# Optimization experiments

Measured on AMD Instinct MI355X. Metric: run time of the kernel, lower is better.

Reference implementation:

```python
import jax, jax.numpy as jnp
import numpy as np

NUM_HOPS = 3
SIGMA = 0.1
EPS = 1e-12  # torch F.normalize default eps


def setup_inputs() -> dict:
    key = jax.random.key(0)
    k1, k2 = jax.random.split(key)
    N, D, E = 50000, 128, 800000
    x = jax.random.normal(k1, (N, D), dtype=jnp.float32)
    edge_index = jax.random.randint(k2, (2, E), 0, N, dtype=jnp.int64)
    return {"x": x, "edge_index": edge_index}


def _l2_normalize(h):
    # matches torch.nn.functional.normalize(x, dim=1)
    n = jnp.linalg.norm(h, axis=1, keepdims=True)
    return h / jnp.maximum(n, EPS)


def reference(x, edge_index):
    N = x.shape[0]
    src, dst = edge_index[0], edge_index[1]
    noise_keys = jax.random.split(jax.random.key(1), NUM_HOPS)

    h = _l2_normalize(x)
    outs = [h]
    for k in range(NUM_HOPS):
        # edge-wise inner-product similarity + sigmoid gate
        e = jnp.sum(h[src] * h[dst], axis=1)          # [E]
        alpha = jax.nn.sigmoid(e)                     # [E]
        # sparse alpha^T @ h == segment-sum over dst of alpha * h[src]
        aggr = jax.ops.segment_sum(alpha[:, None] * h[src], dst, num_segments=N)  # [N, D]
        noised = aggr + SIGMA * jax.random.normal(noise_keys[k], aggr.shape, dtype=x.dtype)
        h = _l2_normalize(noised)
        outs.append(h)
    return jnp.stack(outs)                            # [NUM_HOPS+1, N, D]
```

## Files before the change

kernel.cpp:

```cpp
#include <hip/hip_runtime.h>
#include <cstdint>
#include <cstddef>

#define D 128

typedef float v2f __attribute__((ext_vector_type(2)));

__host__ __device__ inline uint32_t rotl32(uint32_t v, int d) {
  return (v << d) | (v >> (32 - d));
}

__host__ __device__ inline void threefry2x32(uint32_t k0, uint32_t k1,
                                             uint32_t x0, uint32_t x1,
                                             uint32_t* o0, uint32_t* o1) {
  uint32_t k2 = k0 ^ k1 ^ 0x1BD11BDAu;
  x0 += k0; x1 += k1;
#define TF_RND(r) x0 += x1; x1 = rotl32(x1, (r)); x1 ^= x0;
  TF_RND(13) TF_RND(15) TF_RND(26) TF_RND(6)
  x0 += k1; x1 += k2 + 1u;
  TF_RND(17) TF_RND(29) TF_RND(16) TF_RND(24)
  x0 += k2; x1 += k0 + 2u;
  TF_RND(13) TF_RND(15) TF_RND(26) TF_RND(6)
  x0 += k0; x1 += k1 + 3u;
  TF_RND(17) TF_RND(29) TF_RND(16) TF_RND(24)
  x0 += k1; x1 += k2 + 4u;
  TF_RND(13) TF_RND(15) TF_RND(26) TF_RND(6)
  x0 += k2; x1 += k0 + 5u;
#undef TF_RND
  *o0 = x0; *o1 = x1;
}

__device__ inline float erfinv_f32(float x) {
  float w = -log1pf(-x * x);
  float p;
  if (w < 5.0f) {
    w = w - 2.5f;
    p = 2.81022636e-08f;
    p = fmaf(p, w, 3.43273939e-07f);
    p = fmaf(p, w, -3.5233877e-06f);
    p = fmaf(p, w, -4.39150654e-06f);
    p = fmaf(p, w, 0.00021858087f);
    p = fmaf(p, w, -0.00125372503f);
    p = fmaf(p, w, -0.00417768164f);
    p = fmaf(p, w, 0.246640727f);
    p = fmaf(p, w, 1.50140941f);
  } else {
    w = sqrtf(w) - 3.0f;
    p = -0.000200214257f;
    p = fmaf(p, w, 0.000100950558f);
    p = fmaf(p, w, 0.00134934322f);
    p = fmaf(p, w, -0.00367342844f);
    p = fmaf(p, w, 0.00573950773f);
    p = fmaf(p, w, -0.0076224613f);
    p = fmaf(p, w, 0.00943887047f);
    p = fmaf(p, w, 1.00167406f);
    p = fmaf(p, w, 2.83297682f);
  }
  return p * x;
}

__device__ inline float erfinv_fast(float x) {
  float t = fmaf(-x, x, 1.0f);
  float w = -0.693147180559945f * __builtin_amdgcn_logf(t);
  float p;
  if (__builtin_expect(w < 5.0f, 1)) {
    w = w - 2.5f;
    p = 2.81022636e-08f;
    p = fmaf(p, w, 3.43273939e-07f);
    p = fmaf(p, w, -3.5233877e-06f);
    p = fmaf(p, w, -4.39150654e-06f);
    p = fmaf(p, w, 0.00021858087f);
    p = fmaf(p, w, -0.00125372503f);
    p = fmaf(p, w, -0.00417768164f);
    p = fmaf(p, w, 0.246640727f);
    p = fmaf(p, w, 1.50140941f);
  } else {
    w = __builtin_amdgcn_sqrtf(w) - 3.0f;
    p = -0.000200214257f;
    p = fmaf(p, w, 0.000100950558f);
    p = fmaf(p, w, 0.00134934322f);
    p = fmaf(p, w, -0.00367342844f);
    p = fmaf(p, w, 0.00573950773f);
    p = fmaf(p, w, -0.0076224613f);
    p = fmaf(p, w, 0.00943887047f);
    p = fmaf(p, w, 1.00167406f);
    p = fmaf(p, w, 2.83297682f);
  }
  return p * x;
}

__device__ inline float jax_normal_elem(uint32_t k0, uint32_t k1, uint32_t idx) {
  uint32_t o0, o1;
  threefry2x32(k0, k1, 0u, idx, &o0, &o1);
  uint32_t bits = o0 ^ o1;
  float f = __uint_as_float((bits >> 9) | 0x3F800000u) - 1.0f;
  float u = f * 2.0f + (-0.99999994f);
  u = fmaxf(-0.99999994f, u);
  return 1.41421356237309505f * erfinv_f32(u);
}

__device__ inline float jax_normal_fast(uint32_t k0, uint32_t k1, uint32_t idx) {
  uint32_t o0, o1;
  threefry2x32(k0, k1, 0u, idx, &o0, &o1);
  uint32_t bits = o0 ^ o1;
  float f = __uint_as_float((bits >> 9) | 0x3F800000u) - 1.0f;
  float u = f * 2.0f + (-0.99999994f);
  u = fmaxf(-0.99999994f, u);
  return 1.41421356237309505f * erfinv_fast(u);
}

__device__ inline uint32_t f32_to_bf16_rne(float f) {
  uint32_t u = __float_as_uint(f);
  u += 0x7fffu + ((u >> 16) & 1u);
  return u >> 16;
}

__device__ inline void gen_noise8(float* __restrict__ np, size_t NDl, int k,
                                  uint32_t k0, uint32_t k1) {
  size_t base = ((size_t)k * 256 + threadIdx.x) * 8;
  if (base + 8 <= NDl) {
    float vv[8];
#pragma unroll
    for (int i = 0; i < 8; ++i)
      vv[i] = 0.1f * jax_normal_fast(k0, k1, (uint32_t)base + (uint32_t)i);
    float4* q = (float4*)(np + base);
    q[0] = make_float4(vv[0], vv[1], vv[2], vv[3]);
    q[1] = make_float4(vv[4], vv[5], vv[6], vv[7]);
  }
}

__device__ inline bool role_split(int bid, int s, int Z, int* work, int* nz) {
  int k = bid / s;
  int r = bid - k * s;
  if (r == s - 1 && k < Z) { *nz = k; return true; }
  *work = bid - min(k, Z);
  return false;
}

__global__ __launch_bounds__(256) void front_kernel(
    const int* __restrict__ dst, int* __restrict__ counts,
    int* __restrict__ deg_hist, int E4, int E,
    const float* __restrict__ xin, float* __restrict__ out0,
    uint16_t* __restrict__ mir, int N,
    float* __restrict__ noise0, int s, int Z, int nbHist,
    uint32_t k0, uint32_t k1) {
  int w, nz;
  if (role_split(blockIdx.x, s, Z, &w, &nz)) {
    gen_noise8(noise0, (size_t)N * D, nz, k0, k1);
    return;
  }
  if (w < nbHist) {
    if (w == 0) {
      for (int bb = threadIdx.x; bb < 1024; bb += 256) deg_hist[bb] = 0;
    }
    int t = w * 256 + threadIdx.x;
    if (t < E4) {
      int4 d4 = ((const int4*)dst)[t];
      atomicAdd(&counts[d4.x], 1);
      atomicAdd(&counts[d4.y], 1);
      atomicAdd(&counts[d4.z], 1);
      atomicAdd(&counts[d4.w], 1);
    }
    int rem = E4 * 4 + t;
    if (t < E - E4 * 4) atomicAdd(&counts[dst[rem]], 1);
    return;
  }
  int t = (w - nbHist) * 256 + threadIdx.x;
  int row = t >> 6;
  int lane = t & 63;
  if (row >= N) return;
  size_t base = (size_t)row * D + 2 * lane;
  float2 v = *(const float2*)(xin + base);
  float ss = v.x * v.x + v.y * v.y;
#pragma unroll
  for (int off = 32; off > 0; off >>= 1) ss += __shfl_xor(ss, off);
  float denom = fmaxf(sqrtf(ss), 1e-12f);
  float2 o = make_float2(v.x / denom, v.y / denom);
  *(float2*)(out0 + base) = o;
  if (mir) {
    uint32_t wq = f32_to_bf16_rne(o.x) | (f32_to_bf16_rne(o.y) << 16);
    *(uint32_t*)(mir + base) = wq;
  }
}

__global__ __launch_bounds__(256) void scanA_kernel(
    int* __restrict__ counts, int* __restrict__ blocksums,
    int* __restrict__ deg, int* __restrict__ deg_hist, int N) {
  __shared__ int tmp[256];
  __shared__ int lhist[1024];
  for (int b = threadIdx.x; b < 1024; b += 256) lhist[b] = 0;
  int tid = threadIdx.x;
  int i = blockIdx.x * 256 + tid;
  int v = (i < N) ? counts[i] : 0;
  tmp[tid] = v;
  __syncthreads();
  if (i < N) {
    deg[i] = v;
    atomicAdd(&lhist[min(v, 1023)], 1);
  }
  for (int off = 1; off < 256; off <<= 1) {
    int t = (tid >= off) ? tmp[tid - off] : 0;
    __syncthreads();
    tmp[tid] += t;
    __syncthreads();
  }
  if (i < N) counts[i] = tmp[tid] - v;
  if (tid == 255) blocksums[blockIdx.x] = tmp[tid];
  __syncthreads();
  for (int b = threadIdx.x; b < 1024; b += 256) {
    int c = lhist[b];
    if (c) atomicAdd(&deg_hist[b], c);
  }
}

__global__ __launch_bounds__(256) void scanB_kernel(
    int* __restrict__ blocksums, int nb,
    const int* __restrict__ deg_hist, int* __restrict__ deg_cursor) {
  __shared__ int tmp[256];
  int tid = threadIdx.x;
  int v = (tid < nb) ? blocksums[tid] : 0;
  tmp[tid] = v;
  __syncthreads();
  for (int off = 1; off < 256; off <<= 1) {
    int t = (tid >= off) ? tmp[tid - off] : 0;
    __syncthreads();
    tmp[tid] += t;
    __syncthreads();
  }
  if (tid < nb) blocksums[tid] = tmp[tid] - v;
  __syncthreads();
  int loc[4], s = 0;
#pragma unroll
  for (int k = 0; k < 4; ++k) { loc[k] = deg_hist[tid * 4 + k]; s += loc[k]; }
  __syncthreads();
  tmp[tid] = s;
  __syncthreads();
  for (int off = 1; off < 256; off <<= 1) {
    int t = (tid >= off) ? tmp[tid - off] : 0;
    __syncthreads();
    tmp[tid] += t;
    __syncthreads();
  }
  int run = tmp[tid] - s;
#pragma unroll
  for (int k = 0; k < 4; ++k) { deg_cursor[tid * 4 + k] = run; run += loc[k]; }
}

__global__ __launch_bounds__(256) void scanC_kernel(
    int* __restrict__ offsets, int* __restrict__ cursor,
    const int* __restrict__ blocksums, const int* __restrict__ deg,
    int* __restrict__ deg_cursor, int* __restrict__ perm, int N, int E) {
  __shared__ int lhist[1024];
  __shared__ int lbase[1024];
  for (int b = threadIdx.x; b < 1024; b += 256) lhist[b] = 0;
  __syncthreads();
  int i = blockIdx.x * 256 + threadIdx.x;
  int d = 0, lpos = 0;
  if (i < N) {
    int o = offsets[i] + blocksums[blockIdx.x];
    offsets[i] = o;
    cursor[i] = o;
    d = min(deg[i], 1023);
    lpos = atomicAdd(&lhist[d], 1);
  }
  if (i == 0) offsets[N] = E;
  __syncthreads();
  for (int b = threadIdx.x; b < 1024; b += 256) {
    int c = lhist[b];
    lbase[b] = c ? atomicAdd(&deg_cursor[b], c) : 0;
  }
  __syncthreads();
  if (i < N) perm[lbase[d] + lpos] = i;
}

__global__ __launch_bounds__(256) void edgescatter4_kernel(
    const int* __restrict__ src, const int* __restrict__ dst,
    int* __restrict__ cursor, int* __restrict__ sorted_src, int E4, int E) {
  int t = blockIdx.x * blockDim.x + threadIdx.x;
  if (t < E4) {
    int4 d = ((const int4*)dst)[t];
    int4 s = ((const int4*)src)[t];
    sorted_src[atomicAdd(&cursor[d.x], 1)] = s.x;
    sorted_src[atomicAdd(&cursor[d.y], 1)] = s.y;
    sorted_src[atomicAdd(&cursor[d.z], 1)] = s.z;
    sorted_src[atomicAdd(&cursor[d.w], 1)] = s.w;
  }
  int rem = E4 * 4 + t;
  if (t < E - E4 * 4) {
    int d = dst[rem];
    sorted_src[atomicAdd(&cursor[d], 1)] = src[rem];
  }
}

union V8 { float4 v[2]; v2f d[4]; float f[8]; };
union U4B { uint4 v; uint32_t u[4]; };

__device__ inline void hop_edge_pk(const U4B& raw, const V8& b, V8& acc) {
  V8 af;
#pragma unroll
  for (int i = 0; i < 4; ++i) {
    af.f[2 * i] = __uint_as_float(raw.u[i] << 16);
    af.f[2 * i + 1] = __uint_as_float(raw.u[i] & 0xffff0000u);
  }
  v2f p2 = af.d[0] * b.d[0];
#pragma unroll
  for (int q = 1; q < 4; ++q) p2 = __builtin_elementwise_fma(af.d[q], b.d[q], p2);
  float part = p2.x + p2.y;
  part += __shfl_xor(part, 1);
  part += __shfl_xor(part, 2);
  part += __shfl_xor(part, 4);
  part += __shfl_xor(part, 8);
  float alpha = __builtin_amdgcn_rcpf(1.0f + __expf(-part));
  v2f av = { alpha, alpha };
#pragma unroll
  for (int q = 0; q < 4; ++q) acc.d[q] = __builtin_elementwise_fma(av, af.d[q], acc.d[q]);
}

__global__ __launch_bounds__(256, 4) void hop_kernel_bf16_pre(
    const float* __restrict__ hprev, const uint16_t* __restrict__ mprev,
    float* __restrict__ hout, uint16_t* __restrict__ mout,
    const int* __restrict__ offsets, const int* __restrict__ sorted_src,
    const int* __restrict__ perm, const float* __restrict__ noise,
    float* __restrict__ noiseNext, int s, int Z,
    uint32_t nk0, uint32_t nk1, int N, int E) {
  int w, nz;
  if (role_split(blockIdx.x, s, Z, &w, &nz)) {
    gen_noise8(noiseNext, (size_t)N * D, nz, nk0, nk1);
    return;
  }
  int g = w * 16 + (threadIdx.x >> 4);
  int sub = threadIdx.x & 15;
  if (g >= N) return;
  int r = perm[g];
  size_t rbase = (size_t)r * D + sub * 8;

  V8 b;
  {
    const float4* p = (const float4*)(hprev + rbase);
    b.v[0] = p[0]; b.v[1] = p[1];
  }
  V8 acc;
#pragma unroll
  for (int i = 0; i < 8; ++i) acc.f[i] = 0.f;

  int j0 = offsets[r];
  int cnt = offsets[r + 1] - j0;
  int Em1 = E - 1;
  const char* mb = (const char*)mprev + (uint32_t)(sub * 16);

  U4B buf[4];
  int sNext[4];
#pragma unroll
  for (int q = 0; q < 4; ++q) {
    uint32_t sidx = (uint32_t)sorted_src[min(j0 + q, Em1)];
    buf[q].v = *(const uint4*)(mb + (sidx << 8));
  }
#pragma unroll
  for (int q = 0; q < 4; ++q) sNext[q] = sorted_src[min(j0 + 4 + q, Em1)];

  int cnt4 = cnt & ~3;
  for (int i = 0; i < cnt4; i += 4) {
#pragma unroll
    for (int q = 0; q < 4; ++q) {
      hop_edge_pk(buf[q], b, acc);
      buf[q].v = *(const uint4*)(mb + ((uint32_t)sNext[q] << 8));
      sNext[q] = sorted_src[min(j0 + i + 8 + q, Em1)];
    }
  }
  int rem = cnt - cnt4;
#pragma unroll
  for (int q = 0; q < 3; ++q)
    if (q < rem) hop_edge_pk(buf[q], b, acc);

  V8 nzv;
  {
    const float4* p = (const float4*)(noise + rbase);
    nzv.v[0] = p[0]; nzv.v[1] = p[1];
  }
  float ss = 0.f;
#pragma unroll
  for (int i2 = 0; i2 < 8; ++i2) {
    acc.f[i2] += nzv.f[i2];
    ss = fmaf(acc.f[i2], acc.f[i2], ss);
  }
  ss += __shfl_xor(ss, 1);
  ss += __shfl_xor(ss, 2);
  ss += __shfl_xor(ss, 4);
  ss += __shfl_xor(ss, 8);
  float denom = fmaxf(sqrtf(ss), 1e-12f);
  float inv = __builtin_amdgcn_rcpf(denom);
  inv = inv * fmaf(-denom, inv, 2.0f);
#pragma unroll
  for (int i2 = 0; i2 < 8; ++i2) acc.f[i2] *= inv;
  {
    float4* p = (float4*)(hout + rbase);
    p[0] = acc.v[0]; p[1] = acc.v[1];
  }
  if (mout) {
    U4B wq;
#pragma unroll
    for (int i2 = 0; i2 < 4; ++i2)
      wq.u[i2] = f32_to_bf16_rne(acc.f[2 * i2]) |
                 (f32_to_bf16_rne(acc.f[2 * i2 + 1]) << 16);
    *(uint4*)(mout + rbase) = wq.v;
  }
}

__device__ inline void hop_edge(const U4B& raw, const V8& b, V8& acc) {
  V8 af;
#pragma unroll
  for (int i = 0; i < 4; ++i) {
    af.f[2 * i] = __uint_as_float(raw.u[i] << 16);
    af.f[2 * i + 1] = __uint_as_float(raw.u[i] & 0xffff0000u);
  }
  float part = af.f[0] * b.f[0];
#pragma unroll
  for (int q = 1; q < 8; ++q) part = fmaf(af.f[q], b.f[q], part);
  part += __shfl_xor(part, 1);
  part += __shfl_xor(part, 2);
  part += __shfl_xor(part, 4);
  part += __shfl_xor(part, 8);
  float alpha = __builtin_amdgcn_rcpf(1.0f + __expf(-part));
#pragma unroll
  for (int q = 0; q < 8; ++q) acc.f[q] = fmaf(alpha, af.f[q], acc.f[q]);
}

__global__ __launch_bounds__(256, 4) void hop_kernel_bf16(
    const float* __restrict__ hprev, const uint16_t* __restrict__ mprev,
    float* __restrict__ hout, uint16_t* __restrict__ mout,
    const int* __restrict__ offsets, const int* __restrict__ sorted_src,
    const int* __restrict__ perm, int N, int E, uint32_t k0, uint32_t k1) {
  int g = (blockIdx.x * blockDim.x + threadIdx.x) >> 4;
  int sub = threadIdx.x & 15;
  if (g >= N) return;
  int r = perm[g];
  size_t rbase = (size_t)r * D + sub * 8;

  V8 b;
  {
    const float4* p = (const float4*)(hprev + rbase);
    b.v[0] = p[0]; b.v[1] = p[1];
  }
  V8 acc;
#pragma unroll
  for (int i = 0; i < 8; ++i) acc.f[i] = 0.f;

  int j0 = offsets[r];
  int cnt = offsets[r + 1] - j0;
  int Em1 = E - 1;
  const uint16_t* mp = mprev + sub * 8;

  U4B buf[4];
  int sNext[4];
#pragma unroll
  for (int q = 0; q < 4; ++q) {
    int s = sorted_src[min(j0 + q, Em1)];
    buf[q].v = *(const uint4*)(mp + (size_t)s * D);
  }
#pragma unroll
  for (int q = 0; q < 4; ++q) sNext[q] = sorted_src[min(j0 + 4 + q, Em1)];

  int cnt4 = cnt & ~3;
  int i = 0;
  for (; i < cnt4; i += 4) {
#pragma unroll
    for (int q = 0; q < 4; ++q) {
      hop_edge(buf[q], b, acc);
      buf[q].v = *(const uint4*)(mp + (size_t)sNext[q] * D);
      sNext[q] = sorted_src[min(j0 + i + 8 + q, Em1)];
    }
  }
  int rem = cnt - cnt4;
#pragma unroll
  for (int q = 0; q < 3; ++q)
    if (q < rem) hop_edge(buf[q], b, acc);

  uint32_t idx = (uint32_t)rbase;
  float ss = 0.f;
#pragma unroll
  for (int i2 = 0; i2 < 8; ++i2) {
    acc.f[i2] += 0.1f * jax_normal_elem(k0, k1, idx + (uint32_t)i2);
    ss = fmaf(acc.f[i2], acc.f[i2], ss);
  }
  ss += __shfl_xor(ss, 1);
  ss += __shfl_xor(ss, 2);
  ss += __shfl_xor(ss, 4);
  ss += __shfl_xor(ss, 8);
  float denom = fmaxf(sqrtf(ss), 1e-12f);
#pragma unroll
  for (int i2 = 0; i2 < 8; ++i2) acc.f[i2] = acc.f[i2] / denom;
  {
    float4* p = (float4*)(hout + rbase);
    p[0] = acc.v[0]; p[1] = acc.v[1];
  }
  if (mout) {
    U4B w;
#pragma unroll
    for (int i2 = 0; i2 < 4; ++i2)
      w.u[i2] = f32_to_bf16_rne(acc.f[2 * i2]) |
                (f32_to_bf16_rne(acc.f[2 * i2 + 1]) << 16);
    *(uint4*)(mout + rbase) = w.v;
  }
}

union V16 { float4 v[4]; float f[16]; };

__global__ __launch_bounds__(256) void hop_kernel_f32(
    const float* __restrict__ hprev, float* __restrict__ hout,
    const int* __restrict__ offsets, const int* __restrict__ sorted_src,
    const int* __restrict__ perm, int N, uint32_t k0, uint32_t k1) {
  int g = (blockIdx.x * blockDim.x + threadIdx.x) >> 3;
  int sub = threadIdx.x & 7;
  if (g >= N) return;
  int r = perm[g];
  size_t rbase = (size_t)r * D + sub * 16;

  V16 b;
  {
    const float4* p = (const float4*)(hprev + rbase);
    b.v[0] = p[0]; b.v[1] = p[1]; b.v[2] = p[2]; b.v[3] = p[3];
  }
  V16 acc;
#pragma unroll
  for (int i = 0; i < 16; ++i) acc.f[i] = 0.f;

  int j = offsets[r], jhi = offsets[r + 1];
  V16 a;
  if (j < jhi) {
    const float4* p = (const float4*)(hprev + (size_t)sorted_src[j] * D + sub * 16);
    a.v[0] = p[0]; a.v[1] = p[1]; a.v[2] = p[2]; a.v[3] = p[3];
  }
  while (j < jhi) {
    int jn = j + 1;
    V16 an;
    if (jn < jhi) {
      const float4* p = (const float4*)(hprev + (size_t)sorted_src[jn] * D + sub * 16);
      an.v[0] = p[0]; an.v[1] = p[1]; an.v[2] = p[2]; an.v[3] = p[3];
    }
    float part = a.f[0] * b.f[0];
#pragma unroll
    for (int i = 1; i < 16; ++i) part = fmaf(a.f[i], b.f[i], part);
    part += __shfl_xor(part, 1);
    part += __shfl_xor(part, 2);
    part += __shfl_xor(part, 4);
    float alpha = 1.0f / (1.0f + expf(-part));
#pragma unroll
    for (int i = 0; i < 16; ++i) acc.f[i] = fmaf(alpha, a.f[i], acc.f[i]);
    a = an;
    j = jn;
  }

  uint32_t idx = (uint32_t)rbase;
  float ss = 0.f;
#pragma unroll
  for (int i = 0; i < 16; ++i) {
    acc.f[i] += 0.1f * jax_normal_elem(k0, k1, idx + (uint32_t)i);
    ss = fmaf(acc.f[i], acc.f[i], ss);
  }
  ss += __shfl_xor(ss, 1);
  ss += __shfl_xor(ss, 2);
  ss += __shfl_xor(ss, 4);
  float denom = fmaxf(sqrtf(ss), 1e-12f);
#pragma unroll
  for (int i = 0; i < 16; ++i) acc.f[i] = acc.f[i] / denom;
  {
    float4* p = (float4*)(hout + rbase);
    p[0] = acc.v[0]; p[1] = acc.v[1]; p[2] = acc.v[2]; p[3] = acc.v[3];
  }
}

extern "C" void kernel_launch(void* const* d_in, const int* in_sizes, int n_in,
                              void* d_out, int out_size, void* d_ws, size_t ws_size,
                              hipStream_t stream) {
  const float* x = (const float*)d_in[0];
  const int* ei = (const int*)d_in[1];
  int N = in_sizes[0] / D;
  int E = in_sizes[1] / 2;
  const int* src = ei;
  const int* dst = ei + E;
  float* out = (float*)d_out;
  size_t ND = (size_t)N * D;

  int nblocksN = (N + 255) / 256;

  int* offsets = (int*)d_ws;
  int* cursor = offsets + (N + 1);
  int* perm = cursor + N;
  int* deg = perm + N;
  int* deg_hist = deg + N;
  int* deg_cursor = deg_hist + 1024;
  int* blocksums = deg_cursor + 1024;
  int* sorted_src = blocksums + 256;
  size_t intWords = (size_t)(N + 1) + N + N + N + 1024 + 1024 + 256 + E;
  size_t mirOff = (intWords * 4 + 255) & ~(size_t)255;
  size_t needMir = mirOff + 2 * ND * sizeof(uint16_t);
  bool use_bf16 = ws_size >= needMir;
  uint16_t* mir0 = (uint16_t*)((char*)d_ws + mirOff);
  uint16_t* mir1 = mir0 + ND;
  size_t noiseOff = needMir;
  size_t needNoise = noiseOff + 3 * ND * sizeof(float);
  bool use_noise = use_bf16 && ws_size >= needNoise;
  float* noisebuf = (float*)((char*)d_ws + noiseOff);

  uint32_t nk0[3], nk1[3];
  for (int k = 0; k < 3; ++k)
    threefry2x32(0u, 1u, 0u, (uint32_t)k, &nk0[k], &nk1[k]);

  int E4 = E / 4;
  int e4Blocks = (max(E4, E - E4 * 4) + 255) / 256;
  int rowWaveBlocks = (int)(((size_t)N * 64 + 255) / 256);
  int hopBlocks16 = (int)(((size_t)N * 16 + 255) / 256);
  int hopBlocks8 = (int)(((size_t)N * 8 + 255) / 256);

  int nbHist = e4Blocks;
  int nbNorm = rowWaveBlocks;
  int Zn = use_noise ? (int)((ND + 2047) / 2048) : 0;

  int WF = nbHist + nbNorm;
  int TF = WF + Zn;
  int sF = Zn ? max(2, TF / Zn) : 1;
  hipMemsetAsync(offsets, 0, (size_t)(N + 1) * sizeof(int), stream);
  hipLaunchKernelGGL(front_kernel, dim3(TF), dim3(256), 0, stream,
                     dst, offsets, deg_hist, E4, E,
                     x, out, use_bf16 ? mir0 : (uint16_t*)nullptr, N,
                     noisebuf, sF, Zn, nbHist, nk0[0], nk1[0]);
  hipLaunchKernelGGL(scanA_kernel, dim3(nblocksN), dim3(256), 0, stream,
                     offsets, blocksums, deg, deg_hist, N);
  hipLaunchKernelGGL(scanB_kernel, dim3(1), dim3(256), 0, stream,
                     blocksums, nblocksN, deg_hist, deg_cursor);
  hipLaunchKernelGGL(scanC_kernel, dim3(nblocksN), dim3(256), 0, stream,
                     offsets, cursor, blocksums, deg, deg_cursor, perm, N, E);
  hipLaunchKernelGGL(edgescatter4_kernel, dim3(e4Blocks), dim3(256), 0, stream,
                     src, dst, cursor, sorted_src, E4, E);

  if (use_bf16) {
    uint16_t* mirs[4] = {mir0, mir1, mir0, nullptr};
    for (int k = 0; k < 3; ++k) {
      const float* hk = out + (size_t)k * ND;
      float* hk1 = out + (size_t)(k + 1) * ND;
      if (use_noise) {
        int ZH = (k < 2) ? Zn : 0;
        int TH = hopBlocks16 + ZH;
        int sH = ZH ? max(2, TH / ZH) : 1;
        float* nNext = (k < 2) ? (noisebuf + (size_t)(k + 1) * ND) : nullptr;
        uint32_t kn0 = (k < 2) ? nk0[k + 1] : 0u;
        uint32_t kn1 = (k < 2) ? nk1[k + 1] : 0u;
        hipLaunchKernelGGL(hop_kernel_bf16_pre, dim3(TH), dim3(256), 0, stream,
                           hk, mirs[k], hk1, mirs[k + 1], offsets, sorted_src,
                           perm, noisebuf + (size_t)k * ND, nNext, sH, ZH,
                           kn0, kn1, N, E);
      } else {
        hipLaunchKernelGGL(hop_kernel_bf16, dim3(hopBlocks16), dim3(256), 0,
                           stream, hk, mirs[k], hk1, mirs[k + 1], offsets,
                           sorted_src, perm, N, E, nk0[k], nk1[k]);
      }
    }
  } else {
    for (int k = 0; k < 3; ++k) {
      const float* hk = out + (size_t)k * ND;
      float* hk1 = out + (size_t)(k + 1) * ND;
      hipLaunchKernelGGL(hop_kernel_f32, dim3(hopBlocks8), dim3(256), 0, stream,
                         hk, hk1, offsets, sorted_src, perm, N, nk0[k], nk1[k]);
    }
  }
}
```

Measured before the change: 388.8 us.

## Fuse whole pipeline into one cooperative persistent kernel with grid syncs

Replaces the sequence of memset, front, three scan, scatter and three hop launches with a single cooperative mega_kernel that uses grid.sync between phases and grid-stride loops over work units. Noise generation for all three hops is interleaved into the histogram and scatter phases. The aim is to remove per-launch overhead and inter-kernel gaps. In exchange, occupancy is limited to what a cooperative launch allows, and grid-wide barriers are added. The old multi-kernel path is kept as a fallback, with small guards added for the no-noise case.

```diff
diff --git a/kernel.cpp b/kernel.cpp
--- a/kernel.cpp
+++ b/kernel.cpp
@@ -1,6 +1,9 @@
 #include <hip/hip_runtime.h>
+#include <hip/hip_cooperative_groups.h>
 #include <cstdint>
 #include <cstddef>
+
+namespace cg = cooperative_groups;
 
 #define D 128
 
@@ -129,12 +132,325 @@
   }
 }
 
+__device__ inline bool mix_role(int u, int T, int Z, int* work, int* nz) {
+  long long a = (long long)u * Z;
+  int before = (int)(a / T);
+  int after = (int)((a + Z) / T);
+  if (after > before) { *nz = before; return true; }
+  *work = u - before;
+  return false;
+}
+
 __device__ inline bool role_split(int bid, int s, int Z, int* work, int* nz) {
   int k = bid / s;
   int r = bid - k * s;
   if (r == s - 1 && k < Z) { *nz = k; return true; }
   *work = bid - min(k, Z);
   return false;
+}
+
+union V8 { float4 v[2]; v2f d[4]; float f[8]; };
+union U4B { uint4 v; uint32_t u[4]; };
+
+__device__ inline void hop_edge_pk(const U4B& raw, const V8& b, V8& acc) {
+  V8 af;
+#pragma unroll
+  for (int i = 0; i < 4; ++i) {
+    af.f[2 * i] = __uint_as_float(raw.u[i] << 16);
+    af.f[2 * i + 1] = __uint_as_float(raw.u[i] & 0xffff0000u);
+  }
+  v2f p2 = af.d[0] * b.d[0];
+#pragma unroll
+  for (int q = 1; q < 4; ++q) p2 = __builtin_elementwise_fma(af.d[q], b.d[q], p2);
+  float part = p2.x + p2.y;
+  part += __shfl_xor(part, 1);
+  part += __shfl_xor(part, 2);
+  part += __shfl_xor(part, 4);
+  part += __shfl_xor(part, 8);
+  float alpha = __builtin_amdgcn_rcpf(1.0f + __expf(-part));
+  v2f av = { alpha, alpha };
+#pragma unroll
+  for (int q = 0; q < 4; ++q) acc.d[q] = __builtin_elementwise_fma(av, af.d[q], acc.d[q]);
+}
+
+__device__ inline void hop_unit(int g, const float* __restrict__ hprev,
+    const uint16_t* __restrict__ mprev, float* __restrict__ hout,
+    uint16_t* __restrict__ mout, const int* __restrict__ offsets,
+    const int* __restrict__ sorted_src, const int* __restrict__ perm,
+    const float* __restrict__ noise, int N, int E) {
+  int sub = threadIdx.x & 15;
+  if (g >= N) return;
+  int r = perm[g];
+  size_t rbase = (size_t)r * D + sub * 8;
+
+  V8 b;
+  {
+    const float4* p = (const float4*)(hprev + rbase);
+    b.v[0] = p[0]; b.v[1] = p[1];
+  }
+  V8 acc;
+#pragma unroll
+  for (int i = 0; i < 8; ++i) acc.f[i] = 0.f;
+
+  int j0 = offsets[r];
+  int cnt = offsets[r + 1] - j0;
+  int Em1 = E - 1;
+  const char* mb = (const char*)mprev + (uint32_t)(sub * 16);
+
+  U4B buf[4];
+  int sNext[4];
+#pragma unroll
+  for (int q = 0; q < 4; ++q) {
+    uint32_t s = (uint32_t)sorted_src[min(j0 + q, Em1)];
+    buf[q].v = *(const uint4*)(mb + (s << 8));
+  }
+#pragma unroll
+  for (int q = 0; q < 4; ++q) sNext[q] = sorted_src[min(j0 + 4 + q, Em1)];
+
+  int cnt4 = cnt & ~3;
+  for (int i = 0; i < cnt4; i += 4) {
+#pragma unroll
+    for (int q = 0; q < 4; ++q) {
+      hop_edge_pk(buf[q], b, acc);
+      buf[q].v = *(const uint4*)(mb + ((uint32_t)sNext[q] << 8));
+      sNext[q] = sorted_src[min(j0 + i + 8 + q, Em1)];
+    }
+  }
+  int rem = cnt - cnt4;
+#pragma unroll
+  for (int q = 0; q < 3; ++q)
+    if (q < rem) hop_edge_pk(buf[q], b, acc);
+
+  V8 nzv;
+  {
+    const float4* p = (const float4*)(noise + rbase);
+    nzv.v[0] = p[0]; nzv.v[1] = p[1];
+  }
+  float ss = 0.f;
+#pragma unroll
+  for (int i2 = 0; i2 < 8; ++i2) {
+    acc.f[i2] += nzv.f[i2];
+    ss = fmaf(acc.f[i2], acc.f[i2], ss);
+  }
+  ss += __shfl_xor(ss, 1);
+  ss += __shfl_xor(ss, 2);
+  ss += __shfl_xor(ss, 4);
+  ss += __shfl_xor(ss, 8);
+  float denom = fmaxf(sqrtf(ss), 1e-12f);
+  float inv = __builtin_amdgcn_rcpf(denom);
+  inv = inv * fmaf(-denom, inv, 2.0f);
+#pragma unroll
+  for (int i2 = 0; i2 < 8; ++i2) acc.f[i2] *= inv;
+  {
+    float4* p = (float4*)(hout + rbase);
+    p[0] = acc.v[0]; p[1] = acc.v[1];
+  }
+  if (mout) {
+    U4B wq;
+#pragma unroll
+    for (int i2 = 0; i2 < 4; ++i2)
+      wq.u[i2] = f32_to_bf16_rne(acc.f[2 * i2]) |
+                 (f32_to_bf16_rne(acc.f[2 * i2 + 1]) << 16);
+    *(uint4*)(mout + rbase) = wq.v;
+  }
+}
+
+struct MegaArgs {
+  const float* x;
+  const int* src;
+  const int* dst;
+  float* out;
+  int* offsets;
+  int* cursor;
+  int* perm;
+  int* deg;
+  int* deg_hist;
+  int* deg_cursor;
+  int* blocksums;
+  int* sorted_src;
+  uint16_t* mir0;
+  uint16_t* mir1;
+  float* noise;
+  int N, E, E4, nbHist, nbNorm, nbScan, Zn, hopU;
+  uint32_t k0a, k1a, k0b, k1b, k0c, k1c;
+};
+
+__global__ __launch_bounds__(256, 8) void mega_kernel(MegaArgs A) {
+  cg::grid_group grid = cg::this_grid();
+  __shared__ int sh_tmp[256];
+  __shared__ int sh_a[1024];
+  __shared__ int sh_b[1024];
+  const int nb = gridDim.x;
+  const int bid = blockIdx.x;
+  const int tid = threadIdx.x;
+  const size_t NDl = (size_t)A.N * D;
+
+  {
+    int gt = bid * 256 + tid, gs = nb * 256;
+    for (int i = gt; i < A.N + 1; i += gs) A.offsets[i] = 0;
+    for (int i = gt; i < 1024; i += gs) A.deg_hist[i] = 0;
+  }
+  grid.sync();
+
+  {
+    int T = A.nbHist + A.nbNorm + A.Zn;
+    for (int u = bid; u < T; u += nb) {
+      int w, nz;
+      if (mix_role(u, T, A.Zn, &w, &nz)) {
+        gen_noise8(A.noise, NDl, nz, A.k0a, A.k1a);
+      } else if (w < A.nbHist) {
+        int t = w * 256 + tid;
+        if (t < A.E4) {
+          int4 d4 = ((const int4*)A.dst)[t];
+          atomicAdd(&A.offsets[d4.x], 1);
+          atomicAdd(&A.offsets[d4.y], 1);
+          atomicAdd(&A.offsets[d4.z], 1);
+          atomicAdd(&A.offsets[d4.w], 1);
+        }
+        int rem = A.E4 * 4 + t;
+        if (t < A.E - A.E4 * 4) atomicAdd(&A.offsets[A.dst[rem]], 1);
+      } else {
+        int t = (w - A.nbHist) * 256 + tid;
+        int row = t >> 6;
+        int lane = t & 63;
+        if (row < A.N) {
+          size_t base = (size_t)row * D + 2 * lane;
+          float2 v = *(const float2*)(A.x + base);
+          float ss = v.x * v.x + v.y * v.y;
+#pragma unroll
+          for (int off = 32; off > 0; off >>= 1) ss += __shfl_xor(ss, off);
+          float denom = fmaxf(sqrtf(ss), 1e-12f);
+          float2 o = make_float2(v.x / denom, v.y / denom);
+          *(float2*)(A.out + base) = o;
+          uint32_t wq = f32_to_bf16_rne(o.x) | (f32_to_bf16_rne(o.y) << 16);
+          *(uint32_t*)(A.mir0 + base) = wq;
+        }
+      }
+    }
+  }
+  grid.sync();
+
+  for (int vb = bid; vb < A.nbScan; vb += nb) {
+    for (int b2 = tid; b2 < 1024; b2 += 256) sh_a[b2] = 0;
+    int i = vb * 256 + tid;
+    int v = (i < A.N) ? A.offsets[i] : 0;
+    sh_tmp[tid] = v;
+    __syncthreads();
+    if (i < A.N) {
+      A.deg[i] = v;
+      atomicAdd(&sh_a[min(v, 1023)], 1);
+    }
+    for (int off = 1; off < 256; off <<= 1) {
+      int t2 = (tid >= off) ? sh_tmp[tid - off] : 0;
+      __syncthreads();
+      sh_tmp[tid] += t2;
+      __syncthreads();
+    }
+    if (i < A.N) A.offsets[i] = sh_tmp[tid] - v;
+    if (tid == 255) A.blocksums[vb] = sh_tmp[tid];
+    __syncthreads();
+    for (int b2 = tid; b2 < 1024; b2 += 256) {
+      int c = sh_a[b2];
+      if (c) atomicAdd(&A.deg_hist[b2], c);
+    }
+    __syncthreads();
+  }
+  grid.sync();
+
+  if (bid == 0) {
+    int v = (tid < A.nbScan) ? A.blocksums[tid] : 0;
+    sh_tmp[tid] = v;
+    __syncthreads();
+    for (int off = 1; off < 256; off <<= 1) {
+      int t2 = (tid >= off) ? sh_tmp[tid - off] : 0;
+      __syncthreads();
+      sh_tmp[tid] += t2;
+      __syncthreads();
+    }
+    if (tid < A.nbScan) A.blocksums[tid] = sh_tmp[tid] - v;
+    __syncthreads();
+    int loc[4], s = 0;
+#pragma unroll
+    for (int k = 0; k < 4; ++k) { loc[k] = A.deg_hist[tid * 4 + k]; s += loc[k]; }
+    __syncthreads();
+    sh_tmp[tid] = s;
+    __syncthreads();
+    for (int off = 1; off < 256; off <<= 1) {
+      int t2 = (tid >= off) ? sh_tmp[tid - off] : 0;
+      __syncthreads();
+      sh_tmp[tid] += t2;
+      __syncthreads();
+    }
+    int run = sh_tmp[tid] - s;
+#pragma unroll
+    for (int k = 0; k < 4; ++k) { A.deg_cursor[tid * 4 + k] = run; run += loc[k]; }
+  }
+  grid.sync();
+
+  for (int vb = bid; vb < A.nbScan; vb += nb) {
+    for (int b2 = tid; b2 < 1024; b2 += 256) sh_a[b2] = 0;
+    __syncthreads();
+    int i = vb * 256 + tid;
+    int d2 = 0, lpos = 0;
+    if (i < A.N) {
+      int o = A.offsets[i] + A.blocksums[vb];
+      A.offsets[i] = o;
+      A.cursor[i] = o;
+      d2 = min(A.deg[i], 1023);
+      lpos = atomicAdd(&sh_a[d2], 1);
+    }
+    if (i == 0) A.offsets[A.N] = A.E;
+    __syncthreads();
+    for (int b2 = tid; b2 < 1024; b2 += 256) {
+      int c = sh_a[b2];
+      sh_b[b2] = c ? atomicAdd(&A.deg_cursor[b2], c) : 0;
+    }
+    __syncthreads();
+    if (i < A.N) A.perm[sh_b[d2] + lpos] = i;
+    __syncthreads();
+  }
+  grid.sync();
+
+  {
+    int Zs = 2 * A.Zn;
+    int T = A.nbHist + Zs;
+    for (int u = bid; u < T; u += nb) {
+      int w, nz;
+      if (mix_role(u, T, Zs, &w, &nz)) {
+        if (nz < A.Zn) gen_noise8(A.noise + NDl, NDl, nz, A.k0b, A.k1b);
+        else gen_noise8(A.noise + 2 * NDl, NDl, nz - A.Zn, A.k0c, A.k1c);
+      } else {
+        int t = w * 256 + tid;
+        if (t < A.E4) {
+          int4 d4 = ((const int4*)A.dst)[t];
+          int4 s4 = ((const int4*)A.src)[t];
+          A.sorted_src[atomicAdd(&A.cursor[d4.x], 1)] = s4.x;
+          A.sorted_src[atomicAdd(&A.cursor[d4.y], 1)] = s4.y;
+          A.sorted_src[atomicAdd(&A.cursor[d4.z], 1)] = s4.z;
+          A.sorted_src[atomicAdd(&A.cursor[d4.w], 1)] = s4.w;
+        }
+        int rem = A.E4 * 4 + t;
+        if (t < A.E - A.E4 * 4) {
+          int dd = A.dst[rem];
+          A.sorted_src[atomicAdd(&A.cursor[dd], 1)] = A.src[rem];
+        }
+      }
+    }
+  }
+  grid.sync();
+
+  for (int u = bid; u < A.hopU; u += nb)
+    hop_unit(u * 16 + (tid >> 4), A.out, A.mir0, A.out + NDl, A.mir1,
+             A.offsets, A.sorted_src, A.perm, A.noise, A.N, A.E);
+  grid.sync();
+  for (int u = bid; u < A.hopU; u += nb)
+    hop_unit(u * 16 + (tid >> 4), A.out + NDl, A.mir1, A.out + 2 * NDl, A.mir0,
+             A.offsets, A.sorted_src, A.perm, A.noise + NDl, A.N, A.E);
+  grid.sync();
+  for (int u = bid; u < A.hopU; u += nb)
+    hop_unit(u * 16 + (tid >> 4), A.out + 2 * NDl, A.mir0, A.out + 3 * NDl,
+             (uint16_t*)nullptr, A.offsets, A.sorted_src, A.perm,
+             A.noise + 2 * NDl, A.N, A.E);
 }
 
 __global__ __launch_bounds__(256) void front_kernel(
@@ -145,10 +461,11 @@
     float* __restrict__ noise0, int s, int Z, int nbHist,
     uint32_t k0, uint32_t k1) {
   int w, nz;
-  if (role_split(blockIdx.x, s, Z, &w, &nz)) {
+  if (Z > 0 && role_split(blockIdx.x, s, Z, &w, &nz)) {
     gen_noise8(noise0, (size_t)N * D, nz, k0, k1);
     return;
   }
+  if (Z == 0) w = blockIdx.x;
   if (w < nbHist) {
     if (w == 0) {
       for (int bb = threadIdx.x; bb < 1024; bb += 256) deg_hist[bb] = 0;
@@ -292,30 +609,6 @@
   }
 }
 
-union V8 { float4 v[2]; v2f d[4]; float f[8]; };
-union U4B { uint4 v; uint32_t u[4]; };
-
-__device__ inline void hop_edge_pk(const U4B& raw, const V8& b, V8& acc) {
-  V8 af;
-#pragma unroll
-  for (int i = 0; i < 4; ++i) {
-    af.f[2 * i] = __uint_as_float(raw.u[i] << 16);
-    af.f[2 * i + 1] = __uint_as_float(raw.u[i] & 0xffff0000u);
-  }
-  v2f p2 = af.d[0] * b.d[0];
-#pragma unroll
-  for (int q = 1; q < 4; ++q) p2 = __builtin_elementwise_fma(af.d[q], b.d[q], p2);
-  float part = p2.x + p2.y;
-  part += __shfl_xor(part, 1);
-  part += __shfl_xor(part, 2);
-  part += __shfl_xor(part, 4);
-  part += __shfl_xor(part, 8);
-  float alpha = __builtin_amdgcn_rcpf(1.0f + __expf(-part));
-  v2f av = { alpha, alpha };
-#pragma unroll
-  for (int q = 0; q < 4; ++q) acc.d[q] = __builtin_elementwise_fma(av, af.d[q], acc.d[q]);
-}
-
 __global__ __launch_bounds__(256, 4) void hop_kernel_bf16_pre(
     const float* __restrict__ hprev, const uint16_t* __restrict__ mprev,
     float* __restrict__ hout, uint16_t* __restrict__ mout,
@@ -324,183 +617,13 @@
     float* __restrict__ noiseNext, int s, int Z,
     uint32_t nk0, uint32_t nk1, int N, int E) {
   int w, nz;
-  if (role_split(blockIdx.x, s, Z, &w, &nz)) {
+  if (Z > 0 && role_split(blockIdx.x, s, Z, &w, &nz)) {
     gen_noise8(noiseNext, (size_t)N * D, nz, nk0, nk1);
     return;
   }
-  int g = w * 16 + (threadIdx.x >> 4);
-  int sub = threadIdx.x & 15;
-  if (g >= N) return;
-  int r = perm[g];
-  size_t rbase = (size_t)r * D + sub * 8;
-
-  V8 b;
-  {
-    const float4* p = (const float4*)(hprev + rbase);
-    b.v[0] = p[0]; b.v[1] = p[1];
-  }
-  V8 acc;
-#pragma unroll
-  for (int i = 0; i < 8; ++i) acc.f[i] = 0.f;
-
-  int j0 = offsets[r];
-  int cnt = offsets[r + 1] - j0;
-  int Em1 = E - 1;
-  const char* mb = (const char*)mprev + (uint32_t)(sub * 16);
-
-  U4B buf[4];
-  int sNext[4];
-#pragma unroll
-  for (int q = 0; q < 4; ++q) {
-    uint32_t sidx = (uint32_t)sorted_src[min(j0 + q, Em1)];
-    buf[q].v = *(const uint4*)(mb + (sidx << 8));
-  }
-#pragma unroll
-  for (int q = 0; q < 4; ++q) sNext[q] = sorted_src[min(j0 + 4 + q, Em1)];
-
-  int cnt4 = cnt & ~3;
-  for (int i = 0; i < cnt4; i += 4) {
-#pragma unroll
-    for (int q = 0; q < 4; ++q) {
-      hop_edge_pk(buf[q], b, acc);
-      buf[q].v = *(const uint4*)(mb + ((uint32_t)sNext[q] << 8));
-      sNext[q] = sorted_src[min(j0 + i + 8 + q, Em1)];
-    }
-  }
-  int rem = cnt - cnt4;
-#pragma unroll
-  for (int q = 0; q < 3; ++q)
-    if (q < rem) hop_edge_pk(buf[q], b, acc);
-
-  V8 nzv;
-  {
-    const float4* p = (const float4*)(noise + rbase);
-    nzv.v[0] = p[0]; nzv.v[1] = p[1];
-  }
-  float ss = 0.f;
-#pragma unroll
-  for (int i2 = 0; i2 < 8; ++i2) {
-    acc.f[i2] += nzv.f[i2];
-    ss = fmaf(acc.f[i2], acc.f[i2], ss);
-  }
-  ss += __shfl_xor(ss, 1);
-  ss += __shfl_xor(ss, 2);
-  ss += __shfl_xor(ss, 4);
-  ss += __shfl_xor(ss, 8);
-  float denom = fmaxf(sqrtf(ss), 1e-12f);
-  float inv = __builtin_amdgcn_rcpf(denom);
-  inv = inv * fmaf(-denom, inv, 2.0f);
-#pragma unroll
-  for (int i2 = 0; i2 < 8; ++i2) acc.f[i2] *= inv;
-  {
-    float4* p = (float4*)(hout + rbase);
-    p[0] = acc.v[0]; p[1] = acc.v[1];
-  }
-  if (mout) {
-    U4B wq;
-#pragma unroll
-    for (int i2 = 0; i2 < 4; ++i2)
-      wq.u[i2] = f32_to_bf16_rne(acc.f[2 * i2]) |
-                 (f32_to_bf16_rne(acc.f[2 * i2 + 1]) << 16);
-    *(uint4*)(mout + rbase) = wq.v;
-  }
-}
-
-__device__ inline void hop_edge(const U4B& raw, const V8& b, V8& acc) {
-  V8 af;
-#pragma unroll
-  for (int i = 0; i < 4; ++i) {
-    af.f[2 * i] = __uint_as_float(raw.u[i] << 16);
-    af.f[2 * i + 1] = __uint_as_float(raw.u[i] & 0xffff0000u);
-  }
-  float part = af.f[0] * b.f[0];
-#pragma unroll
-  for (int q = 1; q < 8; ++q) part = fmaf(af.f[q], b.f[q], part);
-  part += __shfl_xor(part, 1);
-  part += __shfl_xor(part, 2);
-  part += __shfl_xor(part, 4);
-  part += __shfl_xor(part, 8);
-  float alpha = __builtin_amdgcn_rcpf(1.0f + __expf(-part));
-#pragma unroll
-  for (int q = 0; q < 8; ++q) acc.f[q] = fmaf(alpha, af.f[q], acc.f[q]);
-}
-
-__global__ __launch_bounds__(256, 4) void hop_kernel_bf16(
-    const float* __restrict__ hprev, const uint16_t* __restrict__ mprev,
-    float* __restrict__ hout, uint16_t* __restrict__ mout,
-    const int* __restrict__ offsets, const int* __restrict__ sorted_src,
-    const int* __restrict__ perm, int N, int E, uint32_t k0, uint32_t k1) {
-  int g = (blockIdx.x * blockDim.x + threadIdx.x) >> 4;
-  int sub = threadIdx.x & 15;
-  if (g >= N) return;
-  int r = perm[g];
-  size_t rbase = (size_t)r * D + sub * 8;
-
-  V8 b;
-  {
-    const float4* p = (const float4*)(hprev + rbase);
-    b.v[0] = p[0]; b.v[1] = p[1];
-  }
-  V8 acc;
-#pragma unroll
-  for (int i = 0; i < 8; ++i) acc.f[i] = 0.f;
-
-  int j0 = offsets[r];
-  int cnt = offsets[r + 1] - j0;
-  int Em1 = E - 1;
-  const uint16_t* mp = mprev + sub * 8;
-
-  U4B buf[4];
-  int sNext[4];
-#pragma unroll
-  for (int q = 0; q < 4; ++q) {
-    int s = sorted_src[min(j0 + q, Em1)];
-    buf[q].v = *(const uint4*)(mp + (size_t)s * D);
-  }
-#pragma unroll
-  for (int q = 0; q < 4; ++q) sNext[q] = sorted_src[min(j0 + 4 + q, Em1)];
-
-  int cnt4 = cnt & ~3;
-  int i = 0;
-  for (; i < cnt4; i += 4) {
-#pragma unroll
-    for (int q = 0; q < 4; ++q) {
-      hop_edge(buf[q], b, acc);
-      buf[q].v = *(const uint4*)(mp + (size_t)sNext[q] * D);
-      sNext[q] = sorted_src[min(j0 + i + 8 + q, Em1)];
-    }
-  }
-  int rem = cnt - cnt4;
-#pragma unroll
-  for (int q = 0; q < 3; ++q)
-    if (q < rem) hop_edge(buf[q], b, acc);
-
-  uint32_t idx = (uint32_t)rbase;
-  float ss = 0.f;
-#pragma unroll
-  for (int i2 = 0; i2 < 8; ++i2) {
-    acc.f[i2] += 0.1f * jax_normal_elem(k0, k1, idx + (uint32_t)i2);
-    ss = fmaf(acc.f[i2], acc.f[i2], ss);
-  }
-  ss += __shfl_xor(ss, 1);
-  ss += __shfl_xor(ss, 2);
-  ss += __shfl_xor(ss, 4);
-  ss += __shfl_xor(ss, 8);
-  float denom = fmaxf(sqrtf(ss), 1e-12f);
-#pragma unroll
-  for (int i2 = 0; i2 < 8; ++i2) acc.f[i2] = acc.f[i2] / denom;
-  {
-    float4* p = (float4*)(hout + rbase);
-    p[0] = acc.v[0]; p[1] = acc.v[1];
-  }
-  if (mout) {
-    U4B w;
-#pragma unroll
-    for (int i2 = 0; i2 < 4; ++i2)
-      w.u[i2] = f32_to_bf16_rne(acc.f[2 * i2]) |
-                (f32_to_bf16_rne(acc.f[2 * i2 + 1]) << 16);
-    *(uint4*)(mout + rbase) = w.v;
-  }
+  if (Z == 0) w = blockIdx.x;
+  hop_unit(w * 16 + (threadIdx.x >> 4), hprev, mprev, hout, mout,
+           offsets, sorted_src, perm, noise, N, E);
 }
 
 union V16 { float4 v[4]; float f[16]; };
@@ -611,16 +734,52 @@
   int rowWaveBlocks = (int)(((size_t)N * 64 + 255) / 256);
   int hopBlocks16 = (int)(((size_t)N * 16 + 255) / 256);
   int hopBlocks8 = (int)(((size_t)N * 8 + 255) / 256);
+  int Zn = use_noise ? (int)((ND + 2047) / 2048) : 0;
+
+  static int s_nb = -2;
+  if (s_nb == -2) {
+    s_nb = -1;
+    int devId = 0;
+    if (hipGetDevice(&devId) == hipSuccess) {
+      hipDeviceProp_t prop;
+      if (hipGetDeviceProperties(&prop, devId) == hipSuccess &&
+          prop.cooperativeLaunch) {
+        int maxB = 0;
+        if (hipOccupancyMaxActiveBlocksPerMultiprocessor(&maxB, mega_kernel,
+                                                         256, 0) == hipSuccess &&
+            maxB > 0) {
+          long long g = (long long)maxB * prop.multiProcessorCount;
+          s_nb = (int)(g > 4096 ? 4096 : g);
+        }
+      }
+    }
+  }
+
+  bool try_mega = use_noise && nblocksN <= 256 && s_nb > 0;
+  if (try_mega) {
+    MegaArgs A;
+    A.x = x; A.src = src; A.dst = dst; A.out = out;
+    A.offsets = offsets; A.cursor = cursor; A.perm = perm; A.deg = deg;
+    A.deg_hist = deg_hist; A.deg_cursor = deg_cursor; A.blocksums = blocksums;
+    A.sorted_src = sorted_src; A.mir0 = mir0; A.mir1 = mir1; A.noise = noisebuf;
+    A.N = N; A.E = E; A.E4 = E4; A.nbHist = e4Blocks; A.nbNorm = rowWaveBlocks;
+    A.nbScan = nblocksN; A.Zn = Zn; A.hopU = (N + 15) / 16;
+    A.k0a = nk0[0]; A.k1a = nk1[0];
+    A.k0b = nk0[1]; A.k1b = nk1[1];
+    A.k0c = nk0[2]; A.k1c = nk1[2];
+    void* args[] = { &A };
+    hipError_t cerr = hipLaunchCooperativeKernel(mega_kernel, dim3(s_nb),
+                                                 dim3(256), args, 0, stream);
+    if (cerr == hipSuccess) return;
+  }
 
   int nbHist = e4Blocks;
   int nbNorm = rowWaveBlocks;
-  int Zn = use_noise ? (int)((ND + 2047) / 2048) : 0;
-
   int WF = nbHist + nbNorm;
   int TF = WF + Zn;
   int sF = Zn ? max(2, TF / Zn) : 1;
   hipMemsetAsync(offsets, 0, (size_t)(N + 1) * sizeof(int), stream);
-  hipLaunchKernelGGL(front_kernel, dim3(TF), dim3(256), 0, stream,
+  hipLaunchKernelGGL(front_kernel, dim3(Zn ? TF : WF), dim3(256), 0, stream,
                      dst, offsets, deg_hist, E4, E,
                      x, out, use_bf16 ? mir0 : (uint16_t*)nullptr, N,
                      noisebuf, sF, Zn, nbHist, nk0[0], nk1[0]);
@@ -633,27 +792,22 @@
   hipLaunchKernelGGL(edgescatter4_kernel, dim3(e4Blocks), dim3(256), 0, stream,
                      src, dst, cursor, sorted_src, E4, E);
 
-  if (use_bf16) {
+  if (use_bf16 && use_noise) {
     uint16_t* mirs[4] = {mir0, mir1, mir0, nullptr};
     for (int k = 0; k < 3; ++k) {
       const float* hk = out + (size_t)k * ND;
       float* hk1 = out + (size_t)(k + 1) * ND;
-      if (use_noise) {
-        int ZH = (k < 2) ? Zn : 0;
-        int TH = hopBlocks16 + ZH;
-        int sH = ZH ? max(2, TH / ZH) : 1;
-        float* nNext = (k < 2) ? (noisebuf + (size_t)(k + 1) * ND) : nullptr;
-        uint32_t kn0 = (k < 2) ? nk0[k + 1] : 0u;
-        uint32_t kn1 = (k < 2) ? nk1[k + 1] : 0u;
-        hipLaunchKernelGGL(hop_kernel_bf16_pre, dim3(TH), dim3(256), 0, stream,
-                           hk, mirs[k], hk1, mirs[k + 1], offsets, sorted_src,
-                           perm, noisebuf + (size_t)k * ND, nNext, sH, ZH,
-                           kn0, kn1, N, E);
-      } else {
-        hipLaunchKernelGGL(hop_kernel_bf16, dim3(hopBlocks16), dim3(256), 0,
-                           stream, hk, mirs[k], hk1, mirs[k + 1], offsets,
-                           sorted_src, perm, N, E, nk0[k], nk1[k]);
-      }
+      int ZH = (k < 2) ? Zn : 0;
+      int TH = hopBlocks16 + ZH;
+      int sH = ZH ? max(2, TH / ZH) : 1;
+      float* nNext = (k < 2) ? (noisebuf + (size_t)(k + 1) * ND) : nullptr;
+      uint32_t kn0 = (k < 2) ? nk0[k + 1] : 0u;
+      uint32_t kn1 = (k < 2) ? nk1[k + 1] : 0u;
+      hipLaunchKernelGGL(hop_kernel_bf16_pre, dim3(ZH ? TH : hopBlocks16),
+                         dim3(256), 0, stream, hk, mirs[k], hk1, mirs[k + 1],
+                         offsets, sorted_src, perm,
+                         noisebuf + (size_t)k * ND, nNext, sH, ZH,
+                         kn0, kn1, N, E);
     }
   } else {
     for (int k = 0; k < 3; ++k) {
```

Measured after the change: 1.309 ms. 3.37x slower.
